# Performance work log

Hardware: AMD Instinct MI355X
Metric: run time of the kernel (lower is better)

The kernel has to match this reference:

```python
import jax, jax.numpy as jnp
import numpy as np

NUM_EXPERTS = 8
TOP_K = 2
CAPACITY_FACTOR = 1.25


def setup_inputs() -> dict:
    key = jax.random.key(0)
    ks = jax.random.split(key, 5)
    B, S, D, H, E = 4, 2048, 1024, 2048, NUM_EXPERTS
    scale = 0.02
    return {
        "x": jax.random.normal(ks[0], (B, S, D), dtype=jnp.float32),
        "gate_w": jax.random.normal(ks[1], (E, D), dtype=jnp.float32) * scale,
        "gate_proj_w": jax.random.normal(ks[2], (E, H, D), dtype=jnp.float32) * scale,
        "up_proj_w": jax.random.normal(ks[3], (E, H, D), dtype=jnp.float32) * scale,
        "down_proj_w": jax.random.normal(ks[4], (E, D, H), dtype=jnp.float32) * scale,
    }


def reference(x, gate_w, gate_proj_w, up_proj_w, down_proj_w):
    B, S, D = x.shape
    E, K = NUM_EXPERTS, TOP_K
    T = B * S
    xf = x.reshape(T, D)

    # Router: softmax over expert logits, then top-k (eval mode: no aux loss)
    logits = xf @ gate_w.T                      # (T, E)
    probs = jax.nn.softmax(logits, axis=-1)
    top_p, top_i = jax.lax.top_k(probs, K)      # (T, K)
    w = top_p / (jnp.sum(top_p, axis=-1, keepdims=True) + 1e-9)  # (T, K)

    # Capacity drop: per (k, expert), keep only the first `capacity` tokens
    # in token order (matches torch loop which truncates nonzero indices).
    capacity = int(CAPACITY_FACTOR * T / E)
    oh = jax.nn.one_hot(top_i, E, dtype=jnp.int32)        # (T, K, E)
    rank = jnp.cumsum(oh, axis=0) - 1                     # rank within (k, e)
    my_rank = jnp.sum(rank * oh, axis=-1)                 # (T, K)
    keep = (my_rank < capacity).astype(w.dtype)

    # Combined per-token per-expert weight (dropped tokens get 0)
    comb = jnp.einsum("tk,tke->te", w * keep, oh.astype(w.dtype))  # (T, E)

    # Per-expert dense SwiGLU; zero-weight tokens contribute nothing,
    # which matches the masked gather/scatter-add of the original.
    out = jnp.zeros_like(xf)
    for e in range(E):
        g = jax.nn.silu(xf @ gate_proj_w[e].T)   # (T, H)
        u = xf @ up_proj_w[e].T                  # (T, H)
        y = (g * u) @ down_proj_w[e].T           # (T, D)
        out = out + comb[:, e:e + 1] * y
    return out.reshape(B, S, D)
```

## Files before the change

### kernel.cpp

```cpp
#include <hip/hip_runtime.h>
#include <hip/hip_bf16.h>
#include <stdint.h>

#define T_TOK 8192
#define D_DIM 1024
#define H_DIM 2048
#define E_NUM 8
#define CAP   1280
#define CAP2  2560
#define MT_K  10

#define BM 128
#define BN 128
#define BN_GU 64
#define BK 32

#define ROUTE_BLKS (T_TOK / 4)
#define CONV_BLKS  4096

typedef __attribute__((ext_vector_type(8))) short short8;
typedef __attribute__((ext_vector_type(4))) float float4v;
typedef __attribute__((address_space(1))) const unsigned int gu32;
typedef __attribute__((address_space(3))) unsigned int lu32;

static __device__ __forceinline__ unsigned short f2bf(float f) {
    unsigned int u = __float_as_uint(f);
    unsigned int r = (u + 0x7FFFu + ((u >> 16) & 1u)) >> 16;
    return (unsigned short)r;
}

static __device__ __forceinline__ void store4bf(unsigned short* d, float4 v) {
    union { unsigned short u[4]; uint2 q; } pk;
    pk.u[0] = f2bf(v.x); pk.u[1] = f2bf(v.y);
    pk.u[2] = f2bf(v.z); pk.u[3] = f2bf(v.w);
    *(uint2*)d = pk.q;
}

__global__ __launch_bounds__(256) void prep_k(
    const float* __restrict__ x, const float* __restrict__ gw,
    int* __restrict__ topi, float* __restrict__ topw,
    unsigned short* __restrict__ xbf,
    const float* __restrict__ wg, const float* __restrict__ wu,
    const float* __restrict__ wd,
    unsigned short* __restrict__ wgbf, unsigned short* __restrict__ wubf,
    unsigned short* __restrict__ wdbf) {
    if (blockIdx.x < ROUTE_BLKS) {
        const int t = blockIdx.x * 4 + (threadIdx.x >> 6);
        const int lane = threadIdx.x & 63;
        const float* xr = x + (size_t)t * D_DIM;
        unsigned short* xbr = xbf + (size_t)t * D_DIM;

        float p[E_NUM];
#pragma unroll
        for (int e = 0; e < E_NUM; ++e) p[e] = 0.f;
#pragma unroll
        for (int c = 0; c < 4; ++c) {
            const int idx = c * 256 + lane * 4;
            const float4 xv = *(const float4*)(xr + idx);
            store4bf(xbr + idx, xv);
#pragma unroll
            for (int e = 0; e < E_NUM; ++e) {
                const float4 gv = *(const float4*)(gw + e * D_DIM + idx);
                p[e] += xv.x * gv.x + xv.y * gv.y + xv.z * gv.z + xv.w * gv.w;
            }
        }
#pragma unroll
        for (int e = 0; e < E_NUM; ++e) {
            float v = p[e];
#pragma unroll
            for (int off = 32; off >= 1; off >>= 1) v += __shfl_xor(v, off);
            p[e] = v;
        }
        if (lane == 0) {
            float mx = p[0];
#pragma unroll
            for (int e = 1; e < E_NUM; ++e) mx = fmaxf(mx, p[e]);
            float pe[E_NUM]; float s = 0.f;
#pragma unroll
            for (int e = 0; e < E_NUM; ++e) { pe[e] = expf(p[e] - mx); s += pe[e]; }
            const float inv = 1.f / s;
            int i0 = 0;
#pragma unroll
            for (int e = 1; e < E_NUM; ++e) if (pe[e] > pe[i0]) i0 = e;
            int i1 = -1;
#pragma unroll
            for (int e = 0; e < E_NUM; ++e) {
                if (e == i0) continue;
                if (i1 < 0 || pe[e] > pe[i1]) i1 = e;
            }
            const float p0 = pe[i0] * inv, p1 = pe[i1] * inv;
            const float wn = 1.f / (p0 + p1 + 1e-9f);
            topi[t * 2 + 0] = i0; topi[t * 2 + 1] = i1;
            topw[t * 2 + 0] = p0 * wn; topw[t * 2 + 1] = p1 * wn;
        }
    } else {
        const int W4 = E_NUM * H_DIM * D_DIM / 4;
        const int total = 3 * W4;
        const int stride = CONV_BLKS * 256;
        for (int i = (blockIdx.x - ROUTE_BLKS) * 256 + threadIdx.x; i < total;
             i += stride) {
            const float* s; unsigned short* d; int j;
            if (i < W4)          { s = wg; d = wgbf; j = i; }
            else if (i < 2 * W4) { s = wu; d = wubf; j = i - W4; }
            else                 { s = wd; d = wdbf; j = i - 2 * W4; }
            store4bf(d + (size_t)j * 4, ((const float4*)s)[j]);
        }
    }
}

__global__ __launch_bounds__(256) void router_k(
    const float* __restrict__ x, const float* __restrict__ gw,
    int* __restrict__ topi, float* __restrict__ topw,
    unsigned short* __restrict__ xbf) {
    const int t = blockIdx.x * 4 + (threadIdx.x >> 6);
    const int lane = threadIdx.x & 63;
    const float* xr = x + (size_t)t * D_DIM;
    unsigned short* xbr = xbf + (size_t)t * D_DIM;

    float p[E_NUM];
#pragma unroll
    for (int e = 0; e < E_NUM; ++e) p[e] = 0.f;
#pragma unroll
    for (int c = 0; c < 4; ++c) {
        const int idx = c * 256 + lane * 4;
        const float4 xv = *(const float4*)(xr + idx);
        store4bf(xbr + idx, xv);
#pragma unroll
        for (int e = 0; e < E_NUM; ++e) {
            const float4 gv = *(const float4*)(gw + e * D_DIM + idx);
            p[e] += xv.x * gv.x + xv.y * gv.y + xv.z * gv.z + xv.w * gv.w;
        }
    }
#pragma unroll
    for (int e = 0; e < E_NUM; ++e) {
        float v = p[e];
#pragma unroll
        for (int off = 32; off >= 1; off >>= 1) v += __shfl_xor(v, off);
        p[e] = v;
    }
    if (lane == 0) {
        float mx = p[0];
#pragma unroll
        for (int e = 1; e < E_NUM; ++e) mx = fmaxf(mx, p[e]);
        float pe[E_NUM]; float s = 0.f;
#pragma unroll
        for (int e = 0; e < E_NUM; ++e) { pe[e] = expf(p[e] - mx); s += pe[e]; }
        const float inv = 1.f / s;
        int i0 = 0;
#pragma unroll
        for (int e = 1; e < E_NUM; ++e) if (pe[e] > pe[i0]) i0 = e;
        int i1 = -1;
#pragma unroll
        for (int e = 0; e < E_NUM; ++e) {
            if (e == i0) continue;
            if (i1 < 0 || pe[e] > pe[i1]) i1 = e;
        }
        const float p0 = pe[i0] * inv, p1 = pe[i1] * inv;
        const float wn = 1.f / (p0 + p1 + 1e-9f);
        topi[t * 2 + 0] = i0; topi[t * 2 + 1] = i1;
        topw[t * 2 + 0] = p0 * wn; topw[t * 2 + 1] = p1 * wn;
    }
}

__global__ __launch_bounds__(1024) void assign_k(
    const int* __restrict__ topi, const float* __restrict__ topw,
    int* __restrict__ tok_list, float* __restrict__ w_list,
    int* __restrict__ cnt) {
    __shared__ unsigned char topiL[T_TOK * 2];
    __shared__ int kept[2][E_NUM];
    const int tid = threadIdx.x;
    const int wid = tid >> 6, lane = tid & 63;
    const int k = wid >> 3, e = wid & 7;
    const uint64_t lt = (1ull << lane) - 1ull;

    for (int i = tid; i < T_TOK * 2 / 4; i += 1024) {
        const int4 v = ((const int4*)topi)[i];
        uchar4 b;
        b.x = (unsigned char)v.x; b.y = (unsigned char)v.y;
        b.z = (unsigned char)v.z; b.w = (unsigned char)v.w;
        ((uchar4*)topiL)[i] = b;
    }
    __syncthreads();

    int total = 0;
    for (int base = 0; base < T_TOK; base += 64) {
        const int idx = topiL[(base + lane) * 2 + k];
        total += __popcll(__ballot(idx == e));
    }
    if (lane == 0) {
        const int kc = min(total, CAP);
        kept[k][e] = kc;
        cnt[e * 2 + k] = kc;
    }
    __syncthreads();
    const int myBase = e * CAP2 + k * CAP;

    int running = 0, keptRun = 0;
    for (int base = 0; base < T_TOK; base += 64) {
        const int t = base + lane;
        const bool pred = (topiL[t * 2 + k] == e);
        const uint64_t m = __ballot(pred);
        const int rank = running + __popcll(m & lt);
        const bool keep = pred && (rank < CAP);
        const uint64_t km = __ballot(keep);
        if (keep) {
            const int slot = myBase + keptRun + __popcll(km & lt);
            tok_list[slot] = t;
            w_list[slot] = topw[t * 2 + k];
        }
        running += __popcll(m);
        keptRun += __popcll(km);
    }
    __syncthreads();
    for (int s = tid; s < E_NUM * CAP2; s += 1024) {
        const int ee = s / CAP2;
        const int rem = s - ee * CAP2;
        const int kk = rem / CAP, ls = rem - kk * CAP;
        if (ls >= kept[kk][ee]) { tok_list[s] = 0; w_list[s] = 0.f; }
    }
}

__global__ __launch_bounds__(256, 4) void gateup_bf_k(
    const unsigned short* __restrict__ xbf,
    const unsigned short* __restrict__ wgbf, const unsigned short* __restrict__ wubf,
    const int* __restrict__ tok_list, const int* __restrict__ cnt,
    unsigned short* __restrict__ h_ws, int e0) {
    const int ez = blockIdx.z;
    const int e = e0 + ez;
    const int kk = blockIdx.y / MT_K;
    const int m0 = (blockIdx.y - kk * MT_K) * BM;
    if (m0 >= cnt[e * 2 + kk]) return;
    const int n0 = blockIdx.x * BN_GU;
    const int sbase = e * CAP2 + kk * CAP + m0;
    const size_t hbase = (size_t)ez * CAP2 + kk * CAP + m0;

    __shared__ __align__(1024) unsigned short smem[16384];

    const int tid = threadIdx.x, wid = tid >> 6, lane = tid & 63;

    const unsigned short* gsrc[8];
    int ldsoff[8];
#pragma unroll
    for (int i = 0; i < 8; ++i) {
        const int f = (wid * 8 + i) * 64 + lane;
        const unsigned short* g;
        if (f < 1024) {
            const int r = f >> 3, c = (f & 7) ^ (r & 7);
            const int tok = tok_list[sbase + r];
            g = xbf + (size_t)tok * D_DIM + c * 8;
        } else if (f < 1536) {
            const int fr = f - 1024;
            const int r = fr >> 3, c = (fr & 7) ^ (r & 7);
            g = wgbf + ((size_t)e * H_DIM + n0 + r) * D_DIM + c * 8;
        } else {
            const int fr = f - 1536;
            const int r = fr >> 3, c = (fr & 7) ^ (r & 7);
            g = wubf + ((size_t)e * H_DIM + n0 + r) * D_DIM + c * 8;
        }
        gsrc[i] = g;
        ldsoff[i] = (wid * 8 + i) * 1024;
    }

    float4v accg[4][2], accu[4][2];
#pragma unroll
    for (int i = 0; i < 4; ++i)
#pragma unroll
        for (int j = 0; j < 2; ++j) {
            accg[i][j] = (float4v){0.f, 0.f, 0.f, 0.f};
            accu[i][j] = (float4v){0.f, 0.f, 0.f, 0.f};
        }

    const int wm = (wid & 1) * 64;
    const int wn = (wid >> 1) * 32;
    const int frow = lane & 15;
    const int quad = lane >> 4;

    for (int k0 = 0; k0 < D_DIM; k0 += 64) {
#pragma unroll
        for (int i = 0; i < 8; ++i)
            __builtin_amdgcn_global_load_lds(
                (gu32*)(gsrc[i] + k0),
                (lu32*)((char*)smem + ldsoff[i]), 16, 0, 0);
        __syncthreads();

#pragma unroll
        for (int s = 0; s < 2; ++s) {
            const int c = s * 4 + quad;
            short8 af[4], bgf[2], buf[2];
#pragma unroll
            for (int i = 0; i < 4; ++i) {
                const int row = wm + i * 16 + frow;
                af[i] = *(const short8*)&smem[(row * 8 + (c ^ (row & 7))) * 8];
            }
#pragma unroll
            for (int j = 0; j < 2; ++j) {
                const int row = wn + j * 16 + frow;
                bgf[j] = *(const short8*)&smem[8192 + (row * 8 + (c ^ (row & 7))) * 8];
                buf[j] = *(const short8*)&smem[12288 + (row * 8 + (c ^ (row & 7))) * 8];
            }
#pragma unroll
            for (int i = 0; i < 4; ++i)
#pragma unroll
                for (int j = 0; j < 2; ++j) {
                    accg[i][j] = __builtin_amdgcn_mfma_f32_16x16x32_bf16(af[i], bgf[j], accg[i][j], 0, 0, 0);
                    accu[i][j] = __builtin_amdgcn_mfma_f32_16x16x32_bf16(af[i], buf[j], accu[i][j], 0, 0, 0);
                }
        }
        __syncthreads();
    }

    const int col = lane & 15, rbase = (lane >> 4) * 4;
#pragma unroll
    for (int i = 0; i < 4; ++i)
#pragma unroll
        for (int j = 0; j < 2; ++j)
#pragma unroll
            for (int r = 0; r < 4; ++r) {
                const float g = accg[i][j][r];
                const float u = accu[i][j][r];
                const float hv = (g / (1.f + __expf(-g))) * u;
                const int m = wm + i * 16 + rbase + r;
                const int n = wn + j * 16 + col;
                h_ws[(hbase + m) * H_DIM + (n0 + n)] = f2bf(hv);
            }
}

__global__ __launch_bounds__(256, 3) void down_bf_k(
    const unsigned short* __restrict__ h_ws, const unsigned short* __restrict__ wdbf,
    const int* __restrict__ tok_list, const float* __restrict__ w_list,
    const int* __restrict__ cnt, float* __restrict__ out, int e0, int kk) {
    const int ez = blockIdx.z;
    const int e = e0 + ez;
    const int m0 = blockIdx.y * BM;
    const int nkept = cnt[e * 2 + kk];
    if (m0 >= nkept) return;
    const int n0 = blockIdx.x * BN;
    const int sbase = e * CAP2 + kk * CAP + m0;
    const size_t hbase = (size_t)ez * CAP2 + kk * CAP + m0;

    __shared__ __align__(1024) unsigned short smem[16384];
    __shared__ int tokL[BM];
    __shared__ float wL[BM];

    const int tid = threadIdx.x, wid = tid >> 6, lane = tid & 63;
    if (tid < BM) {
        tokL[tid] = tok_list[sbase + tid];
        wL[tid] = w_list[sbase + tid];
    }

    const unsigned short* gsrc[8];
    int ldsoff[8];
#pragma unroll
    for (int i = 0; i < 8; ++i) {
        const int f = (wid * 8 + i) * 64 + lane;
        const unsigned short* g;
        if (f < 1024) {
            const int r = f >> 3, c = (f & 7) ^ (r & 7);
            g = h_ws + (hbase + r) * H_DIM + c * 8;
        } else {
            const int fr = f - 1024;
            const int r = fr >> 3, c = (fr & 7) ^ (r & 7);
            g = wdbf + ((size_t)e * D_DIM + n0 + r) * H_DIM + c * 8;
        }
        gsrc[i] = g;
        ldsoff[i] = (wid * 8 + i) * 1024;
    }

    float4v acc[4][4];
#pragma unroll
    for (int i = 0; i < 4; ++i)
#pragma unroll
        for (int j = 0; j < 4; ++j) acc[i][j] = (float4v){0.f, 0.f, 0.f, 0.f};

    const int wm = (wid & 1) * 64, wn = (wid >> 1) * 64;
    const int frow = lane & 15;
    const int quad = lane >> 4;

    for (int k0 = 0; k0 < H_DIM; k0 += 64) {
#pragma unroll
        for (int i = 0; i < 8; ++i)
            __builtin_amdgcn_global_load_lds(
                (gu32*)(gsrc[i] + k0),
                (lu32*)((char*)smem + ldsoff[i]), 16, 0, 0);
        __syncthreads();

#pragma unroll
        for (int s = 0; s < 2; ++s) {
            const int c = s * 4 + quad;
            short8 af[4], bf[4];
#pragma unroll
            for (int i = 0; i < 4; ++i) {
                const int row = wm + i * 16 + frow;
                af[i] = *(const short8*)&smem[(row * 8 + (c ^ (row & 7))) * 8];
            }
#pragma unroll
            for (int j = 0; j < 4; ++j) {
                const int row = wn + j * 16 + frow;
                bf[j] = *(const short8*)&smem[8192 + (row * 8 + (c ^ (row & 7))) * 8];
            }
#pragma unroll
            for (int i = 0; i < 4; ++i)
#pragma unroll
                for (int j = 0; j < 4; ++j)
                    acc[i][j] = __builtin_amdgcn_mfma_f32_16x16x32_bf16(af[i], bf[j], acc[i][j], 0, 0, 0);
        }
        __syncthreads();
    }

    const int col = lane & 15, rbase = (lane >> 4) * 4;
#pragma unroll
    for (int i = 0; i < 4; ++i)
#pragma unroll
        for (int r = 0; r < 4; ++r) {
            const int m = wm + i * 16 + rbase + r;
            if (m0 + m >= nkept) continue;
            const float wRow = wL[m];
            float* orow = out + (size_t)tokL[m] * D_DIM + n0;
#pragma unroll
            for (int j = 0; j < 4; ++j) {
                const int n = j * 16 + wn + col;
                const float v = acc[i][j][r] * wRow;
                if (kk == 0) orow[n] = v;
                else         orow[n] += v;
            }
        }
}

__global__ __launch_bounds__(256, 2) void gateup_legacy_k(
    const float* __restrict__ x,
    const float* __restrict__ wg_all, const float* __restrict__ wu_all,
    const int* __restrict__ tok_list, const int* __restrict__ cnt,
    unsigned short* __restrict__ h_ws, int e0) {
    const int ez = blockIdx.z;
    const int e = e0 + ez;
    const int kk = blockIdx.y / MT_K;
    const int m0 = (blockIdx.y - kk * MT_K) * BM;
    if (m0 >= cnt[e * 2 + kk]) return;
    const int n0 = blockIdx.x * BN;
    const int sbase = e * CAP2 + kk * CAP + m0;
    const size_t hbase = (size_t)ez * CAP2 + kk * CAP + m0;

    __shared__ __align__(16) unsigned short As[BM][BK];
    __shared__ __align__(16) unsigned short Bg[BN][BK];
    __shared__ __align__(16) unsigned short Bu[BN][BK];
    __shared__ int tokL[BM];

    const int tid = threadIdx.x;
    if (tid < BM) tokL[tid] = tok_list[sbase + tid];
    __syncthreads();

    const float* wg = wg_all + (size_t)e * H_DIM * D_DIM;
    const float* wu = wu_all + (size_t)e * H_DIM * D_DIM;

    const float* aSrc[4]; const float* gSrc[4]; const float* uSrc[4];
    unsigned short* aDst[4]; unsigned short* gDst[4]; unsigned short* uDst[4];
#pragma unroll
    for (int it = 0; it < 4; ++it) {
        const int fid = it * 256 + tid;
        const int row = fid >> 3;
        const int c4 = (fid & 7) * 4;
        aSrc[it] = x + (size_t)tokL[row] * D_DIM + c4;
        gSrc[it] = wg + (size_t)(n0 + row) * D_DIM + c4;
        uSrc[it] = wu + (size_t)(n0 + row) * D_DIM + c4;
        aDst[it] = &As[row][c4];
        gDst[it] = &Bg[row][c4];
        uDst[it] = &Bu[row][c4];
    }

    float4v accg[4][4], accu[4][4];
#pragma unroll
    for (int i = 0; i < 4; ++i)
#pragma unroll
        for (int j = 0; j < 4; ++j) {
            accg[i][j] = (float4v){0.f, 0.f, 0.f, 0.f};
            accu[i][j] = (float4v){0.f, 0.f, 0.f, 0.f};
        }

    const int wid = tid >> 6, lane = tid & 63;
    const int wm = (wid & 1) * 64, wn = (wid >> 1) * 64;
    const int frow = lane & 15;
    const int fk = (lane >> 4) * 8;

    for (int k0 = 0; k0 < D_DIM; k0 += BK) {
#pragma unroll
        for (int it = 0; it < 4; ++it) {
            store4bf(aDst[it], *(const float4*)(aSrc[it] + k0));
            store4bf(gDst[it], *(const float4*)(gSrc[it] + k0));
            store4bf(uDst[it], *(const float4*)(uSrc[it] + k0));
        }
        __syncthreads();
        short8 af[4], bgf[4], buf[4];
#pragma unroll
        for (int i = 0; i < 4; ++i)
            af[i] = *(const short8*)&As[wm + i * 16 + frow][fk];
#pragma unroll
        for (int j = 0; j < 4; ++j) {
            bgf[j] = *(const short8*)&Bg[wn + j * 16 + frow][fk];
            buf[j] = *(const short8*)&Bu[wn + j * 16 + frow][fk];
        }
#pragma unroll
        for (int i = 0; i < 4; ++i)
#pragma unroll
            for (int j = 0; j < 4; ++j) {
                accg[i][j] = __builtin_amdgcn_mfma_f32_16x16x32_bf16(af[i], bgf[j], accg[i][j], 0, 0, 0);
                accu[i][j] = __builtin_amdgcn_mfma_f32_16x16x32_bf16(af[i], buf[j], accu[i][j], 0, 0, 0);
            }
        __syncthreads();
    }

    const int col = lane & 15, rbase = (lane >> 4) * 4;
#pragma unroll
    for (int i = 0; i < 4; ++i)
#pragma unroll
        for (int j = 0; j < 4; ++j)
#pragma unroll
            for (int r = 0; r < 4; ++r) {
                const float g = accg[i][j][r];
                const float u = accu[i][j][r];
                const float hv = (g / (1.f + __expf(-g))) * u;
                const int m = wm + i * 16 + rbase + r;
                const int n = wn + j * 16 + col;
                h_ws[(hbase + m) * H_DIM + (n0 + n)] = f2bf(hv);
            }
}

__global__ __launch_bounds__(256, 2) void down_legacy_k(
    const unsigned short* __restrict__ h_ws, const float* __restrict__ wd_all,
    const int* __restrict__ tok_list, const float* __restrict__ w_list,
    const int* __restrict__ cnt, float* __restrict__ out, int e0) {
    const int ez = blockIdx.z;
    const int e = e0 + ez;
    const int kk = blockIdx.y / MT_K;
    const int m0 = (blockIdx.y - kk * MT_K) * BM;
    if (m0 >= cnt[e * 2 + kk]) return;
    const int n0 = blockIdx.x * BN;
    const int sbase = e * CAP2 + kk * CAP + m0;
    const size_t hbase = (size_t)ez * CAP2 + kk * CAP + m0;

    __shared__ __align__(16) unsigned short As[BM][BK];
    __shared__ __align__(16) unsigned short Bs[BN][BK];
    __shared__ int tokL[BM];
    __shared__ float wL[BM];

    const int tid = threadIdx.x;
    if (tid < BM) {
        tokL[tid] = tok_list[sbase + tid];
        wL[tid] = w_list[sbase + tid];
    }
    __syncthreads();

    const unsigned short* hA = h_ws + hbase * H_DIM;
    const float* wd = wd_all + (size_t)e * D_DIM * H_DIM;

    const unsigned short* aSrc[2]; unsigned short* aDst[2];
#pragma unroll
    for (int it = 0; it < 2; ++it) {
        const int fid = it * 256 + tid;
        const int row = fid >> 2;
        const int c8 = (fid & 3) * 8;
        aSrc[it] = hA + (size_t)row * H_DIM + c8;
        aDst[it] = &As[row][c8];
    }
    const float* bSrc[4]; unsigned short* bDst[4];
#pragma unroll
    for (int it = 0; it < 4; ++it) {
        const int fid = it * 256 + tid;
        const int row = fid >> 3;
        const int c4 = (fid & 7) * 4;
        bSrc[it] = wd + (size_t)(n0 + row) * H_DIM + c4;
        bDst[it] = &Bs[row][c4];
    }

    float4v acc[4][4];
#pragma unroll
    for (int i = 0; i < 4; ++i)
#pragma unroll
        for (int j = 0; j < 4; ++j) acc[i][j] = (float4v){0.f, 0.f, 0.f, 0.f};

    const int wid = tid >> 6, lane = tid & 63;
    const int wm = (wid & 1) * 64, wn = (wid >> 1) * 64;
    const int frow = lane & 15;
    const int fk = (lane >> 4) * 8;

    for (int k0 = 0; k0 < H_DIM; k0 += BK) {
#pragma unroll
        for (int it = 0; it < 2; ++it)
            *(uint4*)aDst[it] = *(const uint4*)(aSrc[it] + k0);
#pragma unroll
        for (int it = 0; it < 4; ++it)
            store4bf(bDst[it], *(const float4*)(bSrc[it] + k0));
        __syncthreads();
        short8 af[4], bf[4];
#pragma unroll
        for (int i = 0; i < 4; ++i)
            af[i] = *(const short8*)&As[wm + i * 16 + frow][fk];
#pragma unroll
        for (int j = 0; j < 4; ++j)
            bf[j] = *(const short8*)&Bs[wn + j * 16 + frow][fk];
#pragma unroll
        for (int i = 0; i < 4; ++i)
#pragma unroll
            for (int j = 0; j < 4; ++j)
                acc[i][j] = __builtin_amdgcn_mfma_f32_16x16x32_bf16(af[i], bf[j], acc[i][j], 0, 0, 0);
        __syncthreads();
    }

    const int col = lane & 15, rbase = (lane >> 4) * 4;
#pragma unroll
    for (int i = 0; i < 4; ++i)
#pragma unroll
        for (int j = 0; j < 4; ++j)
#pragma unroll
            for (int r = 0; r < 4; ++r) {
                const int m = wm + i * 16 + rbase + r;
                const int n = wn + j * 16 + col;
                const float v = acc[i][j][r] * wL[m];
                unsafeAtomicAdd(&out[(size_t)tokL[m] * D_DIM + n0 + n], v);
            }
}

extern "C" void kernel_launch(void* const* d_in, const int* in_sizes, int n_in,
                              void* d_out, int out_size, void* d_ws, size_t ws_size,
                              hipStream_t stream) {
    const float* x        = (const float*)d_in[0];
    const float* gate_w   = (const float*)d_in[1];
    const float* gate_pw  = (const float*)d_in[2];
    const float* up_pw    = (const float*)d_in[3];
    const float* down_pw  = (const float*)d_in[4];
    float* out = (float*)d_out;
    (void)n_in; (void)in_sizes; (void)out_size;

    uint8_t* ws = (uint8_t*)d_ws;
    size_t off = 0;
    int*   topi     = (int*)(ws + off);   off += (size_t)T_TOK * 2 * 4;
    float* topw     = (float*)(ws + off); off += (size_t)T_TOK * 2 * 4;
    int*   tok_list = (int*)(ws + off);   off += (size_t)E_NUM * CAP2 * 4;
    float* w_list   = (float*)(ws + off); off += (size_t)E_NUM * CAP2 * 4;
    int*   cnt      = (int*)(ws + off);   off += 256;
    off = (off + 4095) & ~(size_t)4095;
    const size_t routing_end = off;

    const size_t x_elems = (size_t)T_TOK * D_DIM;
    const size_t w_elems = (size_t)E_NUM * H_DIM * D_DIM;
    unsigned short* xbf  = (unsigned short*)(ws + off); off += x_elems * 2;
    unsigned short* wgbf = (unsigned short*)(ws + off); off += w_elems * 2;
    unsigned short* wubf = (unsigned short*)(ws + off); off += w_elems * 2;
    unsigned short* wdbf = (unsigned short*)(ws + off); off += w_elems * 2;
    const size_t need_base = off;
    const size_t per_e = (size_t)CAP2 * H_DIM * 2;

    hipMemsetAsync(out, 0, (size_t)T_TOK * D_DIM * sizeof(float), stream);

    if (ws_size >= need_base + per_e) {
        unsigned short* h_ws = (unsigned short*)(ws + need_base);
        int chunk = (int)((ws_size - need_base) / per_e);
        if (chunk > E_NUM) chunk = E_NUM;

        prep_k<<<ROUTE_BLKS + CONV_BLKS, 256, 0, stream>>>(
            x, gate_w, topi, topw, xbf,
            gate_pw, up_pw, down_pw, wgbf, wubf, wdbf);
        assign_k<<<1, 1024, 0, stream>>>(topi, topw, tok_list, w_list, cnt);

        for (int e0 = 0; e0 < E_NUM; e0 += chunk) {
            const int ne = (e0 + chunk <= E_NUM) ? chunk : (E_NUM - e0);
            dim3 g1(H_DIM / BN_GU, 2 * MT_K, ne);
            gateup_bf_k<<<g1, 256, 0, stream>>>(xbf, wgbf, wubf, tok_list, cnt, h_ws, e0);
            dim3 g2(D_DIM / BN, MT_K, ne);
            down_bf_k<<<g2, 256, 0, stream>>>(h_ws, wdbf, tok_list, w_list, cnt, out, e0, 0);
            down_bf_k<<<g2, 256, 0, stream>>>(h_ws, wdbf, tok_list, w_list, cnt, out, e0, 1);
        }
    } else {
        unsigned short* h_ws = (unsigned short*)(ws + routing_end);
        int chunk = (ws_size > routing_end) ? (int)((ws_size - routing_end) / per_e) : 0;
        if (chunk > E_NUM) chunk = E_NUM;
        if (chunk < 1) chunk = 1;

        router_k<<<T_TOK / 4, 256, 0, stream>>>(x, gate_w, topi, topw, xbf);
        assign_k<<<1, 1024, 0, stream>>>(topi, topw, tok_list, w_list, cnt);

        for (int e0 = 0; e0 < E_NUM; e0 += chunk) {
            const int ne = (e0 + chunk <= E_NUM) ? chunk : (E_NUM - e0);
            dim3 g1(H_DIM / BN, 2 * MT_K, ne);
            gateup_legacy_k<<<g1, 256, 0, stream>>>(x, gate_pw, up_pw, tok_list, cnt, h_ws, e0);
            dim3 g2(D_DIM / BN, 2 * MT_K, ne);
            down_legacy_k<<<g2, 256, 0, stream>>>(h_ws, down_pw, tok_list, w_list, cnt, out, e0);
        }
    }
}
```

Baseline: 601.5 us.

## Merge down-projection launches using a split second output buffer and combine pass

The two per-slot down-projection launches become a single launch that covers both top-k slots via blockIdx.z. Slot 1 writes into a separate fp32 buffer, so the two slots never race on the same output row, and a final elementwise kernel adds that buffer into the output. This doubles the parallelism of each down launch and removes one launch per chunk. The cost is an extra 32MB memset, an extra combine pass over 64MB of reads, and less workspace left for h_ws, which may reduce the expert chunk size.

```diff
diff --git a/kernel.cpp b/kernel.cpp
--- a/kernel.cpp
+++ b/kernel.cpp
@@ -325,6 +325,120 @@
             }
 }
 
+__global__ __launch_bounds__(256, 3) void down_split_bf_k(
+    const unsigned short* __restrict__ h_ws, const unsigned short* __restrict__ wdbf,
+    const int* __restrict__ tok_list, const float* __restrict__ w_list,
+    const int* __restrict__ cnt, float* __restrict__ out,
+    float* __restrict__ out2, int e0) {
+    const int ez = blockIdx.z >> 1;
+    const int kk = blockIdx.z & 1;
+    const int e = e0 + ez;
+    const int m0 = blockIdx.y * BM;
+    const int nkept = cnt[e * 2 + kk];
+    if (m0 >= nkept) return;
+    const int n0 = blockIdx.x * BN;
+    const int sbase = e * CAP2 + kk * CAP + m0;
+    const size_t hbase = (size_t)ez * CAP2 + kk * CAP + m0;
+
+    __shared__ __align__(1024) unsigned short smem[16384];
+    __shared__ int tokL[BM];
+    __shared__ float wL[BM];
+
+    const int tid = threadIdx.x, wid = tid >> 6, lane = tid & 63;
+    if (tid < BM) {
+        tokL[tid] = tok_list[sbase + tid];
+        wL[tid] = w_list[sbase + tid];
+    }
+
+    const unsigned short* gsrc[8];
+    int ldsoff[8];
+#pragma unroll
+    for (int i = 0; i < 8; ++i) {
+        const int f = (wid * 8 + i) * 64 + lane;
+        const unsigned short* g;
+        if (f < 1024) {
+            const int r = f >> 3, c = (f & 7) ^ (r & 7);
+            g = h_ws + (hbase + r) * H_DIM + c * 8;
+        } else {
+            const int fr = f - 1024;
+            const int r = fr >> 3, c = (fr & 7) ^ (r & 7);
+            g = wdbf + ((size_t)e * D_DIM + n0 + r) * H_DIM + c * 8;
+        }
+        gsrc[i] = g;
+        ldsoff[i] = (wid * 8 + i) * 1024;
+    }
+
+    float4v acc[4][4];
+#pragma unroll
+    for (int i = 0; i < 4; ++i)
+#pragma unroll
+        for (int j = 0; j < 4; ++j) acc[i][j] = (float4v){0.f, 0.f, 0.f, 0.f};
+
+    const int wm = (wid & 1) * 64, wn = (wid >> 1) * 64;
+    const int frow = lane & 15;
+    const int quad = lane >> 4;
+
+    for (int k0 = 0; k0 < H_DIM; k0 += 64) {
+#pragma unroll
+        for (int i = 0; i < 8; ++i)
+            __builtin_amdgcn_global_load_lds(
+                (gu32*)(gsrc[i] + k0),
+                (lu32*)((char*)smem + ldsoff[i]), 16, 0, 0);
+        __syncthreads();
+
+#pragma unroll
+        for (int s = 0; s < 2; ++s) {
+            const int c = s * 4 + quad;
+            short8 af[4], bf[4];
+#pragma unroll
+            for (int i = 0; i < 4; ++i) {
+                const int row = wm + i * 16 + frow;
+                af[i] = *(const short8*)&smem[(row * 8 + (c ^ (row & 7))) * 8];
+            }
+#pragma unroll
+            for (int j = 0; j < 4; ++j) {
+                const int row = wn + j * 16 + frow;
+                bf[j] = *(const short8*)&smem[8192 + (row * 8 + (c ^ (row & 7))) * 8];
+            }
+#pragma unroll
+            for (int i = 0; i < 4; ++i)
+#pragma unroll
+                for (int j = 0; j < 4; ++j)
+                    acc[i][j] = __builtin_amdgcn_mfma_f32_16x16x32_bf16(af[i], bf[j], acc[i][j], 0, 0, 0);
+        }
+        __syncthreads();
+    }
+
+    float* dbuf = kk ? out2 : out;
+    const int col = lane & 15, rbase = (lane >> 4) * 4;
+#pragma unroll
+    for (int i = 0; i < 4; ++i)
+#pragma unroll
+        for (int r = 0; r < 4; ++r) {
+            const int m = wm + i * 16 + rbase + r;
+            if (m0 + m >= nkept) continue;
+            const float wRow = wL[m];
+            float* orow = dbuf + (size_t)tokL[m] * D_DIM + n0;
+#pragma unroll
+            for (int j = 0; j < 4; ++j) {
+                const int n = j * 16 + wn + col;
+                orow[n] = acc[i][j][r] * wRow;
+            }
+        }
+}
+
+__global__ __launch_bounds__(256) void combine_k(
+    float* __restrict__ out, const float* __restrict__ out2) {
+    const int total = T_TOK * D_DIM / 4;
+    const int stride = gridDim.x * 256;
+    for (int i = blockIdx.x * 256 + threadIdx.x; i < total; i += stride) {
+        float4 a = ((float4*)out)[i];
+        const float4 b = ((const float4*)out2)[i];
+        a.x += b.x; a.y += b.y; a.z += b.z; a.w += b.w;
+        ((float4*)out)[i] = a;
+    }
+}
+
 __global__ __launch_bounds__(256, 3) void down_bf_k(
     const unsigned short* __restrict__ h_ws, const unsigned short* __restrict__ wdbf,
     const int* __restrict__ tok_list, const float* __restrict__ w_list,
@@ -647,11 +761,33 @@
     unsigned short* wubf = (unsigned short*)(ws + off); off += w_elems * 2;
     unsigned short* wdbf = (unsigned short*)(ws + off); off += w_elems * 2;
     const size_t need_base = off;
+    const size_t out2_sz = (size_t)T_TOK * D_DIM * 4;
     const size_t per_e = (size_t)CAP2 * H_DIM * 2;
 
     hipMemsetAsync(out, 0, (size_t)T_TOK * D_DIM * sizeof(float), stream);
 
-    if (ws_size >= need_base + per_e) {
+    if (ws_size >= need_base + out2_sz + per_e) {
+        float* out2 = (float*)(ws + need_base);
+        unsigned short* h_ws = (unsigned short*)(ws + need_base + out2_sz);
+        int chunk = (int)((ws_size - need_base - out2_sz) / per_e);
+        if (chunk > E_NUM) chunk = E_NUM;
+
+        hipMemsetAsync(out2, 0, out2_sz, stream);
+        prep_k<<<ROUTE_BLKS + CONV_BLKS, 256, 0, stream>>>(
+            x, gate_w, topi, topw, xbf,
+            gate_pw, up_pw, down_pw, wgbf, wubf, wdbf);
+        assign_k<<<1, 1024, 0, stream>>>(topi, topw, tok_list, w_list, cnt);
+
+        for (int e0 = 0; e0 < E_NUM; e0 += chunk) {
+            const int ne = (e0 + chunk <= E_NUM) ? chunk : (E_NUM - e0);
+            dim3 g1(H_DIM / BN_GU, 2 * MT_K, ne);
+            gateup_bf_k<<<g1, 256, 0, stream>>>(xbf, wgbf, wubf, tok_list, cnt, h_ws, e0);
+            dim3 g2(D_DIM / BN, MT_K, 2 * ne);
+            down_split_bf_k<<<g2, 256, 0, stream>>>(h_ws, wdbf, tok_list, w_list,
+                                                    cnt, out, out2, e0);
+        }
+        combine_k<<<2048, 256, 0, stream>>>(out, out2);
+    } else if (ws_size >= need_base + per_e) {
         unsigned short* h_ws = (unsigned short*)(ws + need_base);
         int chunk = (int)((ws_size - need_base) / per_e);
         if (chunk > E_NUM) chunk = E_NUM;
```

Result: no change. 599.0 us (-0.4%).
